# Kernel optimization log

Hardware: AMD Instinct MI355X
Metric: run time of the kernel (lower is better)

## Reference

```python
import jax, jax.numpy as jnp
import numpy as np

HEADS = 16
D_MODEL = 1024
HEAD_DIM = D_MODEL // HEADS


def setup_inputs() -> dict:
    key = jax.random.key(0)
    ks = jax.random.split(key, 11)
    B, S, D = 2, 2048, D_MODEL
    s = 1.0 / np.sqrt(D)
    inp = {
        'Q': jax.random.normal(ks[0], (B, S, D), jnp.float32),
        'K': jax.random.normal(ks[1], (B, S, D), jnp.float32),
        'V': jax.random.normal(ks[2], (B, S, D), jnp.float32),
        'Wq': jax.random.normal(ks[3], (D, D), jnp.float32) * s,
        'Wk': jax.random.normal(ks[4], (D, D), jnp.float32) * s,
        'Wv': jax.random.normal(ks[5], (D, D), jnp.float32) * s,
        'Wo': jax.random.normal(ks[6], (D, D), jnp.float32) * s,
        'bq': jnp.zeros((D,), jnp.float32),
        'bk': jnp.zeros((D,), jnp.float32),
        'bv': jnp.zeros((D,), jnp.float32),
        'bo': jnp.zeros((D,), jnp.float32),
    }
    return inp


def reference(Q, K, V, Wq, Wk, Wv, Wo, bq, bk, bv, bo):
    B, S, D = Q.shape
    H, Dh = HEADS, HEAD_DIM
    # projections (torch Linear: x @ W.T + b)
    q = (Q @ Wq.T + bq).reshape(B, S, H, Dh).transpose(0, 2, 1, 3)  # [B,H,S,Dh]
    k = (K @ Wk.T + bk).reshape(B, S, H, Dh).transpose(0, 2, 1, 3)
    v = (V @ Wv.T + bv).reshape(B, S, H, Dh).transpose(0, 2, 1, 3)
    # naive scaled dot-product attention, scale = 1/sqrt(head_dim)
    scores = jnp.einsum('bhqd,bhkd->bhqk', q, k) / jnp.sqrt(jnp.float32(Dh))
    attn = jax.nn.softmax(scores, axis=-1)
    out = jnp.einsum('bhqk,bhkd->bhqd', attn, v)
    concat = out.transpose(0, 2, 1, 3).reshape(B, S, D)
    return concat @ Wo.T + bo
```

## Files before the change

### kernel.cpp

```cpp
#include <hip/hip_runtime.h>
#include <hip/hip_bf16.h>


#define SEQ     2048
#define DMODEL  1024
#define NHEADS  16
#define DH      64
#define MROWS   4096
#define M1      (1024*1024)
#define M4      (4*1024*1024)
#define SCQ     0.18033688f

typedef __hip_bfloat16 bf16;
typedef __attribute__((ext_vector_type(8))) short  short8;
typedef __attribute__((ext_vector_type(4))) short  sv4;
typedef __attribute__((ext_vector_type(4))) float  f32x4;

__device__ __forceinline__ bf16  f2b(float x) { return __float2bfloat16(x); }
__device__ __forceinline__ short f2bs(float f) {
    union { bf16 b; short s; } x; x.b = __float2bfloat16(f); return x.s;
}
__device__ __forceinline__ f32x4 mfma16(short8 a, short8 b, f32x4 c) {
    return __builtin_amdgcn_mfma_f32_16x16x32_bf16(a, b, c, 0, 0, 0);
}
__device__ __forceinline__ short8 pk8(float4 a, float4 b) {
    return (short8){f2bs(a.x), f2bs(a.y), f2bs(a.z), f2bs(a.w),
                    f2bs(b.x), f2bs(b.y), f2bs(b.z), f2bs(b.w)};
}
union SV8 { short8 v; sv4 h[2]; };

__global__ __launch_bounds__(256) void cvt_w(
    const float* __restrict__ W0, const float* __restrict__ W1,
    const float* __restrict__ W2, const float* __restrict__ W3,
    bf16* __restrict__ dst)
{
    const int gid = blockIdx.x * 256 + threadIdx.x;
    const int t   = gid >> 17;
    const int off = (gid & 131071) * 8;
    const float* srcs[4] = {W0, W1, W2, W3};
    const float* s = srcs[t] + off;
    float4 a = *(const float4*)s, b = *(const float4*)(s + 4);
    *(short8*)((short*)dst + (size_t)gid * 8) = pk8(a, b);
}

__global__ __launch_bounds__(256) void cvt_3(
    const float* __restrict__ X0, const float* __restrict__ X1,
    const float* __restrict__ X2,
    bf16* __restrict__ D0, bf16* __restrict__ D1, bf16* __restrict__ D2)
{
    const int gid = blockIdx.x * 256 + threadIdx.x;
    const int t   = gid >> 19;
    const int off = (gid & 524287) * 8;
    const float* srcs[3] = {X0, X1, X2};
    bf16*        dsts[3] = {D0, D1, D2};
    const float* s = srcs[t] + off;
    float4 a = *(const float4*)s, b = *(const float4*)(s + 4);
    *(short8*)((short*)dsts[t] + off) = pk8(a, b);
}

__global__ __launch_bounds__(256) void cvt_1(
    const float* __restrict__ X, bf16* __restrict__ D)
{
    const int gid = blockIdx.x * 256 + threadIdx.x;
    const int off = gid * 8;
    float4 a = *(const float4*)(X + off), b = *(const float4*)(X + off + 4);
    *(short8*)((short*)D + off) = pk8(a, b);
}

__device__ __forceinline__ void gemm_body(
    const bf16* __restrict__ A, const bf16* __restrict__ B,
    const float* __restrict__ bias, void* __restrict__ outp,
    int m0, int n0, int mode, int bias_m, float scale)
{
    __shared__ short As[128 * 32];
    __shared__ short Bs[128 * 32];

    const int tid  = threadIdx.x;
    const int lane = tid & 63;
    const int wv   = tid >> 6;
    const int wm   = (wv >> 1) * 64;
    const int wn   = (wv & 1) * 64;
    const int fn   = lane & 15;
    const int fq   = lane >> 4;

    const int srow = lane >> 2;
    const int scol = (lane & 3) * 8;

    const short* Ag = (const short*)A;
    const short* Bg = (const short*)B;

    f32x4 acc[4][4];
#pragma unroll
    for (int i = 0; i < 4; ++i)
#pragma unroll
        for (int j = 0; j < 4; ++j) acc[i][j] = (f32x4){0.f, 0.f, 0.f, 0.f};

    for (int k0 = 0; k0 < DMODEL; k0 += 32) {
#pragma unroll
        for (int i = 0; i < 2; ++i) {
            const int rr = wv * 32 + i * 16;
            const short* ga = Ag + (size_t)(m0 + rr + srow) * DMODEL + k0 + scol;
            const short* gb = Bg + (size_t)(n0 + rr + srow) * DMODEL + k0 + scol;
            __builtin_amdgcn_global_load_lds(
                (const __attribute__((address_space(1))) void*)ga,
                (__attribute__((address_space(3))) void*)(As + rr * 32), 16, 0, 0);
            __builtin_amdgcn_global_load_lds(
                (const __attribute__((address_space(1))) void*)gb,
                (__attribute__((address_space(3))) void*)(Bs + rr * 32), 16, 0, 0);
        }
        __syncthreads();

        short8 af[4], bfr[4];
#pragma unroll
        for (int im = 0; im < 4; ++im)
            af[im] = *(const short8*)(As + (wm + im * 16 + fn) * 32 + fq * 8);
#pragma unroll
        for (int in = 0; in < 4; ++in)
            bfr[in] = *(const short8*)(Bs + (wn + in * 16 + fn) * 32 + fq * 8);
#pragma unroll
        for (int im = 0; im < 4; ++im)
#pragma unroll
            for (int in = 0; in < 4; ++in)
                acc[im][in] = mfma16(af[im], bfr[in], acc[im][in]);
        __syncthreads();
    }

#pragma unroll
    for (int im = 0; im < 4; ++im) {
#pragma unroll
        for (int in = 0; in < 4; ++in) {
#pragma unroll
            for (int r = 0; r < 4; ++r) {
                const int m = m0 + wm + im * 16 + fq * 4 + r;
                const int n = n0 + wn + in * 16 + fn;
                const float c = (acc[im][in][r] + (bias_m ? bias[m] : bias[n])) * scale;
                if (mode == 0) {
                    ((float*)outp)[(size_t)m * DMODEL + n] = c;
                } else if (mode == 1) {
                    const int b = m >> 11, s = m & (SEQ - 1);
                    const int h = n >> 6,  d = n & (DH - 1);
                    ((bf16*)outp)[(((size_t)(b * NHEADS + h) * SEQ) + s) * DH + d] = f2b(c);
                } else {
                    const int h = m >> 6,  d = m & (DH - 1);
                    const int b = n >> 11, s = n & (SEQ - 1);
                    ((bf16*)outp)[(((size_t)(b * NHEADS + h) * DH) + d) * SEQ + s] = f2b(c);
                }
            }
        }
    }
}

__global__ __launch_bounds__(256, 3) void gemm_one(
    const bf16* A, const bf16* B, const float* bias, void* out,
    int mode, int bias_m, float scale)
{
    gemm_body(A, B, bias, out, blockIdx.x * 128, blockIdx.y * 128,
              mode, bias_m, scale);
}

__global__ __launch_bounds__(256, 3) void gemm_qkv(
    const bf16* Qb, const bf16* Kb, const bf16* Vb, const bf16* Wb,
    const float* bq, const float* bk, const float* bv,
    bf16* qp, bf16* kp, bf16* vp)
{
    const int blk = blockIdx.x;
    const int z = blk >> 8, t = blk & 255;
    if (z == 0)
        gemm_body(Qb, Wb,          bq, qp, (t >> 3) * 128, (t & 7) * 128, 1, 0, SCQ);
    else if (z == 1)
        gemm_body(Kb, Wb + M1,     bk, kp, (t >> 3) * 128, (t & 7) * 128, 1, 0, 1.f);
    else
        gemm_body(Wb + 2 * M1, Vb, bv, vp, (t >> 5) * 128, (t & 31) * 128, 2, 1, 1.f);
}

__global__ __launch_bounds__(256) void attn_mfma(
    const bf16* __restrict__ q,
    const bf16* __restrict__ k,
    const bf16* __restrict__ vt,
    bf16* __restrict__ out)
{
    __shared__ short Kt[64 * 64];
    __shared__ short Vt[64 * 64];

    const int tid  = threadIdx.x;
    const int wave = tid >> 6;
    const int lane = tid & 63;
    const int n    = lane & 15;
    const int quad = lane >> 4;

    const int blk = blockIdx.x;
    const int bh  = blk >> 4;
    const int qt  = blk & 15;
    const int q0w = qt * 128 + wave * 32;

    const bf16* qhead = q  + (size_t)bh * SEQ * DH;
    const bf16* khead = k  + (size_t)bh * SEQ * DH;
    const bf16* vhead = vt + (size_t)bh * DH * SEQ;

    short8 qf[2][2];
#pragma unroll
    for (int qg = 0; qg < 2; ++qg) {
        const short* qr = (const short*)(qhead + (size_t)(q0w + qg * 16 + n) * DH);
        qf[qg][0] = *(const short8*)(qr + quad * 8);
        qf[qg][1] = *(const short8*)(qr + 32 + quad * 8);
    }

    f32x4 O[4][2];
#pragma unroll
    for (int gd = 0; gd < 4; ++gd)
#pragma unroll
        for (int qg = 0; qg < 2; ++qg) O[gd][qg] = (f32x4){0.f, 0.f, 0.f, 0.f};
    f32x4 lp[2] = {(f32x4){0.f,0.f,0.f,0.f}, (f32x4){0.f,0.f,0.f,0.f}};

    const int srow = lane >> 3;
    const int schk = (lane & 7) ^ srow;

    for (int kt = 0; kt < SEQ / 64; ++kt) {
        const int kbase = kt * 64;
#pragma unroll
        for (int i = 0; i < 2; ++i) {
            const int r = wave * 16 + i * 8 + srow;
            const char* gk = (const char*)(khead + (size_t)(kbase + r) * DH) + schk * 16;
            const char* gv = (const char*)(vhead + (size_t)r * SEQ + kbase) + schk * 16;
            __builtin_amdgcn_global_load_lds(
                (const __attribute__((address_space(1))) void*)gk,
                (__attribute__((address_space(3))) void*)(Kt + (wave * 16 + i * 8) * 64),
                16, 0, 0);
            __builtin_amdgcn_global_load_lds(
                (const __attribute__((address_space(1))) void*)gv,
                (__attribute__((address_space(3))) void*)(Vt + (wave * 16 + i * 8) * 64),
                16, 0, 0);
        }
        __syncthreads();

        f32x4 st[4][2];
#pragma unroll
        for (int g = 0; g < 4; ++g) {
            const short* kr = Kt + (g * 16 + n) * 64;
            short8 kf0 = *(const short8*)(kr + ((quad     ^ (n & 7)) * 8));
            short8 kf1 = *(const short8*)(kr + (((4 + quad) ^ (n & 7)) * 8));
#pragma unroll
            for (int qg = 0; qg < 2; ++qg) {
                f32x4 s = (f32x4){0.f, 0.f, 0.f, 0.f};
                s = mfma16(kf0, qf[qg][0], s);
                s = mfma16(kf1, qf[qg][1], s);
                st[g][qg] = s;
            }
        }

        short8 bP[2][2];
#pragma unroll
        for (int t = 0; t < 2; ++t) {
#pragma unroll
            for (int qg = 0; qg < 2; ++qg) {
                f32x4 p0, p1;
#pragma unroll
                for (int r = 0; r < 4; ++r) {
                    p0[r] = exp2f(st[2 * t][qg][r]);
                    p1[r] = exp2f(st[2 * t + 1][qg][r]);
                }
                lp[qg] += p0 + p1;
                bP[t][qg] = (short8){f2bs(p0[0]), f2bs(p0[1]), f2bs(p0[2]), f2bs(p0[3]),
                                     f2bs(p1[0]), f2bs(p1[1]), f2bs(p1[2]), f2bs(p1[3])};
            }
        }

#pragma unroll
        for (int gd = 0; gd < 4; ++gd) {
            const short* vr = Vt + (gd * 16 + n) * 64;
#pragma unroll
            for (int t = 0; t < 2; ++t) {
                SV8 va;
                va.h[0] = *(const sv4*)(vr + (((4 * t +     (quad >> 1)) ^ (n & 7)) * 8) + (quad & 1) * 4);
                va.h[1] = *(const sv4*)(vr + (((4 * t + 2 + (quad >> 1)) ^ (n & 7)) * 8) + (quad & 1) * 4);
#pragma unroll
                for (int qg = 0; qg < 2; ++qg)
                    O[gd][qg] = mfma16(va.v, bP[t][qg], O[gd][qg]);
            }
        }
        __syncthreads();
    }

    float inv[2];
#pragma unroll
    for (int qg = 0; qg < 2; ++qg) {
        float l = lp[qg][0] + lp[qg][1] + lp[qg][2] + lp[qg][3];
        l += __shfl_xor(l, 16, 64);
        l += __shfl_xor(l, 32, 64);
        inv[qg] = 1.0f / l;
    }

    const int b = bh >> 4;
    const int h = bh & (NHEADS - 1);
#pragma unroll
    for (int gd = 0; gd < 4; ++gd) {
#pragma unroll
        for (int qg = 0; qg < 2; ++qg) {
            const int s = q0w + qg * 16 + n;
            sv4 o4 = (sv4){f2bs(O[gd][qg][0] * inv[qg]), f2bs(O[gd][qg][1] * inv[qg]),
                           f2bs(O[gd][qg][2] * inv[qg]), f2bs(O[gd][qg][3] * inv[qg])};
            *(sv4*)(out + ((size_t)(b * SEQ + s)) * DMODEL + h * DH + gd * 16 + quad * 4) = o4;
        }
    }
}

extern "C" void kernel_launch(void* const* d_in, const int* in_sizes, int n_in,
                              void* d_out, int out_size, void* d_ws, size_t ws_size,
                              hipStream_t stream) {
    const float* Q  = (const float*)d_in[0];
    const float* K  = (const float*)d_in[1];
    const float* V  = (const float*)d_in[2];
    const float* Wq = (const float*)d_in[3];
    const float* Wk = (const float*)d_in[4];
    const float* Wv = (const float*)d_in[5];
    const float* Wo = (const float*)d_in[6];
    const float* bq = (const float*)d_in[7];
    const float* bk = (const float*)d_in[8];
    const float* bv = (const float*)d_in[9];
    const float* bo = (const float*)d_in[10];

    bf16* kp = (bf16*)d_out;
    bf16* vp = kp + M4;

    dim3 bb(256);
    dim3 gqk(MROWS / 128, DMODEL / 128);
    dim3 gvv(DMODEL / 128, MROWS / 128);

    if (ws_size >= (size_t)40 * 1024 * 1024) {
        bf16* Wb = (bf16*)d_ws;
        bf16* Qb = Wb + M4;
        bf16* Kb = Qb + M4;
        bf16* Vb = Kb + M4;
        bf16* qp = Vb + M4;
        bf16* ao = Qb;

        cvt_w<<<2048, bb, 0, stream>>>(Wq, Wk, Wv, Wo, Wb);
        cvt_3<<<6144, bb, 0, stream>>>(Q, K, V, Qb, Kb, Vb);
        gemm_qkv<<<768, bb, 0, stream>>>(Qb, Kb, Vb, Wb, bq, bk, bv, qp, kp, vp);
        attn_mfma<<<NHEADS * 2 * (SEQ / 128), bb, 0, stream>>>(qp, kp, vp, ao);
        gemm_one<<<gqk, bb, 0, stream>>>(ao, Wb + 3 * M1, bo, d_out, 0, 0, 1.f);
    } else {
        bf16* Wb = (bf16*)d_ws;
        bf16* Xb = Wb + M4;
        bf16* qp = Xb + M4;
        bf16* ao = Xb;

        cvt_w<<<2048, bb, 0, stream>>>(Wq, Wk, Wv, Wo, Wb);
        cvt_1<<<2048, bb, 0, stream>>>(Q, Xb);
        gemm_one<<<gqk, bb, 0, stream>>>(Xb, Wb, bq, qp, 1, 0, SCQ);
        cvt_1<<<2048, bb, 0, stream>>>(K, Xb);
        gemm_one<<<gqk, bb, 0, stream>>>(Xb, Wb + M1, bk, kp, 1, 0, 1.f);
        cvt_1<<<2048, bb, 0, stream>>>(V, Xb);
        gemm_one<<<gvv, bb, 0, stream>>>(Wb + 2 * M1, Xb, bv, vp, 2, 1, 1.f);
        attn_mfma<<<NHEADS * 2 * (SEQ / 128), bb, 0, stream>>>(qp, kp, vp, ao);
        gemm_one<<<gqk, bb, 0, stream>>>(ao, Wb + 3 * M1, bo, d_out, 0, 0, 1.f);
    }
}
```

Before: 260.6 us.

## Merge conversions, permute V layout, use MFMA row sums, XCD-aware attention, narrower final GEMM

```diff
diff --git a/kernel.cpp b/kernel.cpp
--- a/kernel.cpp
+++ b/kernel.cpp
@@ -13,21 +13,43 @@
 
 typedef __hip_bfloat16 bf16;
 typedef __attribute__((ext_vector_type(8))) short  short8;
-typedef __attribute__((ext_vector_type(4))) short  sv4;
 typedef __attribute__((ext_vector_type(4))) float  f32x4;
 
-__device__ __forceinline__ bf16  f2b(float x) { return __float2bfloat16(x); }
-__device__ __forceinline__ short f2bs(float f) {
-    union { bf16 b; short s; } x; x.b = __float2bfloat16(f); return x.s;
-}
+__device__ __forceinline__ bf16 f2b(float x) { return __float2bfloat16(x); }
 __device__ __forceinline__ f32x4 mfma16(short8 a, short8 b, f32x4 c) {
     return __builtin_amdgcn_mfma_f32_16x16x32_bf16(a, b, c, 0, 0, 0);
 }
+__device__ __forceinline__ unsigned pk2(float a, float b) {
+    union { __hip_bfloat162 h; unsigned u; } x;
+    x.h = __float22bfloat162_rn(float2{a, b});
+    return x.u;
+}
 __device__ __forceinline__ short8 pk8(float4 a, float4 b) {
-    return (short8){f2bs(a.x), f2bs(a.y), f2bs(a.z), f2bs(a.w),
-                    f2bs(b.x), f2bs(b.y), f2bs(b.z), f2bs(b.w)};
-}
-union SV8 { short8 v; sv4 h[2]; };
+    union { short8 s; unsigned u[4]; } x;
+    x.u[0] = pk2(a.x, a.y); x.u[1] = pk2(a.z, a.w);
+    x.u[2] = pk2(b.x, b.y); x.u[3] = pk2(b.z, b.w);
+    return x.s;
+}
+
+__global__ __launch_bounds__(256) void cvt_all(
+    const float* __restrict__ Wq, const float* __restrict__ Wk,
+    const float* __restrict__ Wv, const float* __restrict__ Wo,
+    const float* __restrict__ Q,  const float* __restrict__ K,
+    const float* __restrict__ V,  bf16* __restrict__ dst)
+{
+    const size_t gid = (size_t)blockIdx.x * 256 + threadIdx.x;
+    const size_t e0 = gid * 8;
+    const float* s;
+    if (e0 < (size_t)4 * M1) {
+        const float* w[4] = {Wq, Wk, Wv, Wo};
+        s = w[e0 >> 20] + (e0 & (M1 - 1));
+    } else {
+        const float* a[4] = {nullptr, Q, K, V};
+        s = a[e0 >> 22] + (e0 & (M4 - 1));
+    }
+    float4 x = *(const float4*)s, y = *(const float4*)(s + 4);
+    *(short8*)((short*)dst + e0) = pk8(x, y);
+}
 
 __global__ __launch_bounds__(256) void cvt_w(
     const float* __restrict__ W0, const float* __restrict__ W1,
@@ -43,21 +65,6 @@
     *(short8*)((short*)dst + (size_t)gid * 8) = pk8(a, b);
 }
 
-__global__ __launch_bounds__(256) void cvt_3(
-    const float* __restrict__ X0, const float* __restrict__ X1,
-    const float* __restrict__ X2,
-    bf16* __restrict__ D0, bf16* __restrict__ D1, bf16* __restrict__ D2)
-{
-    const int gid = blockIdx.x * 256 + threadIdx.x;
-    const int t   = gid >> 19;
-    const int off = (gid & 524287) * 8;
-    const float* srcs[3] = {X0, X1, X2};
-    bf16*        dsts[3] = {D0, D1, D2};
-    const float* s = srcs[t] + off;
-    float4 a = *(const float4*)s, b = *(const float4*)(s + 4);
-    *(short8*)((short*)dsts[t] + off) = pk8(a, b);
-}
-
 __global__ __launch_bounds__(256) void cvt_1(
     const float* __restrict__ X, bf16* __restrict__ D)
 {
@@ -67,19 +74,21 @@
     *(short8*)((short*)D + off) = pk8(a, b);
 }
 
+template <int BN>
 __device__ __forceinline__ void gemm_body(
     const bf16* __restrict__ A, const bf16* __restrict__ B,
     const float* __restrict__ bias, void* __restrict__ outp,
     int m0, int n0, int mode, int bias_m, float scale)
 {
     __shared__ short As[128 * 32];
-    __shared__ short Bs[128 * 32];
+    __shared__ short Bs[BN * 32];
+    constexpr int NI = BN / 32;
 
     const int tid  = threadIdx.x;
     const int lane = tid & 63;
     const int wv   = tid >> 6;
     const int wm   = (wv >> 1) * 64;
-    const int wn   = (wv & 1) * 64;
+    const int wn   = (wv & 1) * (BN / 2);
     const int fn   = lane & 15;
     const int fq   = lane >> 4;
 
@@ -89,38 +98,42 @@
     const short* Ag = (const short*)A;
     const short* Bg = (const short*)B;
 
-    f32x4 acc[4][4];
+    f32x4 acc[4][NI];
 #pragma unroll
     for (int i = 0; i < 4; ++i)
 #pragma unroll
-        for (int j = 0; j < 4; ++j) acc[i][j] = (f32x4){0.f, 0.f, 0.f, 0.f};
+        for (int j = 0; j < NI; ++j) acc[i][j] = (f32x4){0.f, 0.f, 0.f, 0.f};
 
     for (int k0 = 0; k0 < DMODEL; k0 += 32) {
 #pragma unroll
         for (int i = 0; i < 2; ++i) {
             const int rr = wv * 32 + i * 16;
             const short* ga = Ag + (size_t)(m0 + rr + srow) * DMODEL + k0 + scol;
-            const short* gb = Bg + (size_t)(n0 + rr + srow) * DMODEL + k0 + scol;
             __builtin_amdgcn_global_load_lds(
                 (const __attribute__((address_space(1))) void*)ga,
                 (__attribute__((address_space(3))) void*)(As + rr * 32), 16, 0, 0);
+        }
+#pragma unroll
+        for (int i = 0; i < BN / 64; ++i) {
+            const int rr = wv * (BN / 4) + i * 16;
+            const short* gb = Bg + (size_t)(n0 + rr + srow) * DMODEL + k0 + scol;
             __builtin_amdgcn_global_load_lds(
                 (const __attribute__((address_space(1))) void*)gb,
                 (__attribute__((address_space(3))) void*)(Bs + rr * 32), 16, 0, 0);
         }
         __syncthreads();
 
-        short8 af[4], bfr[4];
+        short8 af[4], bfr[NI];
 #pragma unroll
         for (int im = 0; im < 4; ++im)
             af[im] = *(const short8*)(As + (wm + im * 16 + fn) * 32 + fq * 8);
 #pragma unroll
-        for (int in = 0; in < 4; ++in)
+        for (int in = 0; in < NI; ++in)
             bfr[in] = *(const short8*)(Bs + (wn + in * 16 + fn) * 32 + fq * 8);
 #pragma unroll
         for (int im = 0; im < 4; ++im)
 #pragma unroll
-            for (int in = 0; in < 4; ++in)
+            for (int in = 0; in < NI; ++in)
                 acc[im][in] = mfma16(af[im], bfr[in], acc[im][in]);
         __syncthreads();
     }
@@ -128,7 +141,7 @@
 #pragma unroll
     for (int im = 0; im < 4; ++im) {
 #pragma unroll
-        for (int in = 0; in < 4; ++in) {
+        for (int in = 0; in < NI; ++in) {
 #pragma unroll
             for (int r = 0; r < 4; ++r) {
                 const int m = m0 + wm + im * 16 + fq * 4 + r;
@@ -143,7 +156,9 @@
                 } else {
                     const int h = m >> 6,  d = m & (DH - 1);
                     const int b = n >> 11, s = n & (SEQ - 1);
-                    ((bf16*)outp)[(((size_t)(b * NHEADS + h) * DH) + d) * SEQ + s] = f2b(c);
+                    const int p = s & 31;
+                    const int sp = (s & ~31) | ((p & 12) << 1) | ((p & 16) >> 2) | (p & 3);
+                    ((bf16*)outp)[(((size_t)(b * NHEADS + h) * DH) + d) * SEQ + sp] = f2b(c);
                 }
             }
         }
@@ -154,8 +169,14 @@
     const bf16* A, const bf16* B, const float* bias, void* out,
     int mode, int bias_m, float scale)
 {
-    gemm_body(A, B, bias, out, blockIdx.x * 128, blockIdx.y * 128,
-              mode, bias_m, scale);
+    gemm_body<128>(A, B, bias, out, blockIdx.x * 128, blockIdx.y * 128,
+                   mode, bias_m, scale);
+}
+
+__global__ __launch_bounds__(256, 3) void gemm_fin(
+    const bf16* A, const bf16* B, const float* bias, void* out)
+{
+    gemm_body<64>(A, B, bias, out, blockIdx.x * 128, blockIdx.y * 64, 0, 0, 1.f);
 }
 
 __global__ __launch_bounds__(256, 3) void gemm_qkv(
@@ -166,11 +187,11 @@
     const int blk = blockIdx.x;
     const int z = blk >> 8, t = blk & 255;
     if (z == 0)
-        gemm_body(Qb, Wb,          bq, qp, (t >> 3) * 128, (t & 7) * 128, 1, 0, SCQ);
+        gemm_body<128>(Qb, Wb,          bq, qp, (t >> 3) * 128, (t & 7) * 128, 1, 0, SCQ);
     else if (z == 1)
-        gemm_body(Kb, Wb + M1,     bk, kp, (t >> 3) * 128, (t & 7) * 128, 1, 0, 1.f);
+        gemm_body<128>(Kb, Wb + M1,     bk, kp, (t >> 3) * 128, (t & 7) * 128, 1, 0, 1.f);
     else
-        gemm_body(Wb + 2 * M1, Vb, bv, vp, (t >> 5) * 128, (t & 31) * 128, 2, 1, 1.f);
+        gemm_body<128>(Wb + 2 * M1, Vb, bv, vp, (t >> 5) * 128, (t & 31) * 128, 2, 1, 1.f);
 }
 
 __global__ __launch_bounds__(256) void attn_mfma(
@@ -188,10 +209,12 @@
     const int n    = lane & 15;
     const int quad = lane >> 4;
 
-    const int blk = blockIdx.x;
-    const int bh  = blk >> 4;
-    const int qt  = blk & 15;
-    const int q0w = qt * 128 + wave * 32;
+    const int blk  = blockIdx.x;
+    const int xcd  = blk & 7;
+    const int rest = blk >> 3;
+    const int qt   = rest & 15;
+    const int bh   = ((rest >> 4) << 3) | xcd;
+    const int q0w  = qt * 128 + wave * 32;
 
     const bf16* qhead = q  + (size_t)bh * SEQ * DH;
     const bf16* khead = k  + (size_t)bh * SEQ * DH;
@@ -205,12 +228,15 @@
         qf[qg][1] = *(const short8*)(qr + 32 + quad * 8);
     }
 
+    const short8 onesv = {(short)0x3F80, (short)0x3F80, (short)0x3F80, (short)0x3F80,
+                          (short)0x3F80, (short)0x3F80, (short)0x3F80, (short)0x3F80};
+
     f32x4 O[4][2];
 #pragma unroll
     for (int gd = 0; gd < 4; ++gd)
 #pragma unroll
         for (int qg = 0; qg < 2; ++qg) O[gd][qg] = (f32x4){0.f, 0.f, 0.f, 0.f};
-    f32x4 lp[2] = {(f32x4){0.f,0.f,0.f,0.f}, (f32x4){0.f,0.f,0.f,0.f}};
+    f32x4 lacc[2] = {(f32x4){0.f,0.f,0.f,0.f}, (f32x4){0.f,0.f,0.f,0.f}};
 
     const int srow = lane >> 3;
     const int schk = (lane & 7) ^ srow;
@@ -237,7 +263,7 @@
 #pragma unroll
         for (int g = 0; g < 4; ++g) {
             const short* kr = Kt + (g * 16 + n) * 64;
-            short8 kf0 = *(const short8*)(kr + ((quad     ^ (n & 7)) * 8));
+            short8 kf0 = *(const short8*)(kr + ((quad       ^ (n & 7)) * 8));
             short8 kf1 = *(const short8*)(kr + (((4 + quad) ^ (n & 7)) * 8));
 #pragma unroll
             for (int qg = 0; qg < 2; ++qg) {
@@ -253,15 +279,13 @@
         for (int t = 0; t < 2; ++t) {
 #pragma unroll
             for (int qg = 0; qg < 2; ++qg) {
-                f32x4 p0, p1;
-#pragma unroll
-                for (int r = 0; r < 4; ++r) {
-                    p0[r] = exp2f(st[2 * t][qg][r]);
-                    p1[r] = exp2f(st[2 * t + 1][qg][r]);
-                }
-                lp[qg] += p0 + p1;
-                bP[t][qg] = (short8){f2bs(p0[0]), f2bs(p0[1]), f2bs(p0[2]), f2bs(p0[3]),
-                                     f2bs(p1[0]), f2bs(p1[1]), f2bs(p1[2]), f2bs(p1[3])};
+                union { short8 s8; unsigned u[4]; } bb;
+                bb.u[0] = pk2(exp2f(st[2*t][qg][0]),   exp2f(st[2*t][qg][1]));
+                bb.u[1] = pk2(exp2f(st[2*t][qg][2]),   exp2f(st[2*t][qg][3]));
+                bb.u[2] = pk2(exp2f(st[2*t+1][qg][0]), exp2f(st[2*t+1][qg][1]));
+                bb.u[3] = pk2(exp2f(st[2*t+1][qg][2]), exp2f(st[2*t+1][qg][3]));
+                bP[t][qg] = bb.s8;
+                lacc[qg] = mfma16(onesv, bP[t][qg], lacc[qg]);
             }
         }
 
@@ -270,36 +294,29 @@
             const short* vr = Vt + (gd * 16 + n) * 64;
 #pragma unroll
             for (int t = 0; t < 2; ++t) {
-                SV8 va;
-                va.h[0] = *(const sv4*)(vr + (((4 * t +     (quad >> 1)) ^ (n & 7)) * 8) + (quad & 1) * 4);
-                va.h[1] = *(const sv4*)(vr + (((4 * t + 2 + (quad >> 1)) ^ (n & 7)) * 8) + (quad & 1) * 4);
+                short8 vf = *(const short8*)(vr + (((t * 4 + quad) ^ (n & 7)) * 8));
 #pragma unroll
                 for (int qg = 0; qg < 2; ++qg)
-                    O[gd][qg] = mfma16(va.v, bP[t][qg], O[gd][qg]);
+                    O[gd][qg] = mfma16(vf, bP[t][qg], O[gd][qg]);
             }
         }
         __syncthreads();
     }
 
-    float inv[2];
-#pragma unroll
-    for (int qg = 0; qg < 2; ++qg) {
-        float l = lp[qg][0] + lp[qg][1] + lp[qg][2] + lp[qg][3];
-        l += __shfl_xor(l, 16, 64);
-        l += __shfl_xor(l, 32, 64);
-        inv[qg] = 1.0f / l;
-    }
-
+    const float inv0 = 1.0f / lacc[0][0];
+    const float inv1 = 1.0f / lacc[1][0];
     const int b = bh >> 4;
     const int h = bh & (NHEADS - 1);
 #pragma unroll
     for (int gd = 0; gd < 4; ++gd) {
 #pragma unroll
         for (int qg = 0; qg < 2; ++qg) {
+            const float iv = qg ? inv1 : inv0;
             const int s = q0w + qg * 16 + n;
-            sv4 o4 = (sv4){f2bs(O[gd][qg][0] * inv[qg]), f2bs(O[gd][qg][1] * inv[qg]),
-                           f2bs(O[gd][qg][2] * inv[qg]), f2bs(O[gd][qg][3] * inv[qg])};
-            *(sv4*)(out + ((size_t)(b * SEQ + s)) * DMODEL + h * DH + gd * 16 + quad * 4) = o4;
+            uint2 o;
+            o.x = pk2(O[gd][qg][0] * iv, O[gd][qg][1] * iv);
+            o.y = pk2(O[gd][qg][2] * iv, O[gd][qg][3] * iv);
+            *(uint2*)(out + ((size_t)(b * SEQ + s)) * DMODEL + h * DH + gd * 16 + quad * 4) = o;
         }
     }
 }
@@ -325,23 +342,23 @@
     dim3 bb(256);
     dim3 gqk(MROWS / 128, DMODEL / 128);
     dim3 gvv(DMODEL / 128, MROWS / 128);
+    dim3 gfin(MROWS / 128, DMODEL / 64);
 
     if (ws_size >= (size_t)40 * 1024 * 1024) {
         bf16* Wb = (bf16*)d_ws;
-        bf16* Qb = Wb + M4;
+        bf16* Qb = Wb + 4 * M1;
         bf16* Kb = Qb + M4;
         bf16* Vb = Kb + M4;
         bf16* qp = Vb + M4;
         bf16* ao = Qb;
 
-        cvt_w<<<2048, bb, 0, stream>>>(Wq, Wk, Wv, Wo, Wb);
-        cvt_3<<<6144, bb, 0, stream>>>(Q, K, V, Qb, Kb, Vb);
+        cvt_all<<<8192, bb, 0, stream>>>(Wq, Wk, Wv, Wo, Q, K, V, Wb);
         gemm_qkv<<<768, bb, 0, stream>>>(Qb, Kb, Vb, Wb, bq, bk, bv, qp, kp, vp);
-        attn_mfma<<<NHEADS * 2 * (SEQ / 128), bb, 0, stream>>>(qp, kp, vp, ao);
-        gemm_one<<<gqk, bb, 0, stream>>>(ao, Wb + 3 * M1, bo, d_out, 0, 0, 1.f);
+        attn_mfma<<<512, bb, 0, stream>>>(qp, kp, vp, ao);
+        gemm_fin<<<gfin, bb, 0, stream>>>(ao, Wb + 3 * M1, bo, d_out);
     } else {
         bf16* Wb = (bf16*)d_ws;
-        bf16* Xb = Wb + M4;
+        bf16* Xb = Wb + 4 * M1;
         bf16* qp = Xb + M4;
         bf16* ao = Xb;
 
@@ -352,7 +369,7 @@
         gemm_one<<<gqk, bb, 0, stream>>>(Xb, Wb + M1, bk, kp, 1, 0, 1.f);
         cvt_1<<<2048, bb, 0, stream>>>(V, Xb);
         gemm_one<<<gvv, bb, 0, stream>>>(Wb + 2 * M1, Xb, bv, vp, 2, 1, 1.f);
-        attn_mfma<<<NHEADS * 2 * (SEQ / 128), bb, 0, stream>>>(qp, kp, vp, ao);
-        gemm_one<<<gqk, bb, 0, stream>>>(ao, Wb + 3 * M1, bo, d_out, 0, 0, 1.f);
-    }
-}
+        attn_mfma<<<512, bb, 0, stream>>>(qp, kp, vp, ao);
+        gemm_fin<<<gfin, bb, 0, stream>>>(ao, Wb + 3 * M1, bo, d_out);
+    }
+}
```

Measured after the change: 241.6 us. 1.08x faster.
